# Kernel tuning notes

Measured on AMD Instinct MI355X. Metric: run time of the kernel, lower is better.

## Reference

```python
import jax, jax.numpy as jnp
import numpy as np

D = 1024
ITERATIONS = 2


def setup_inputs() -> dict:
    key = jax.random.key(0)
    ks = jax.random.split(key, 7)
    s = 1.0 / np.sqrt(D)  # PyTorch GRUCell/Linear init scale
    x = jax.random.normal(ks[0], (8, 4096, D), dtype=jnp.float32)
    W_ih = jax.random.uniform(ks[1], (3 * D, D), minval=-s, maxval=s, dtype=jnp.float32)
    W_hh = jax.random.uniform(ks[2], (3 * D, D), minval=-s, maxval=s, dtype=jnp.float32)
    b_ih = jax.random.uniform(ks[3], (3 * D,), minval=-s, maxval=s, dtype=jnp.float32)
    b_hh = jax.random.uniform(ks[4], (3 * D,), minval=-s, maxval=s, dtype=jnp.float32)
    We = jax.random.uniform(ks[5], (1, D), minval=-s, maxval=s, dtype=jnp.float32)
    be = jax.random.uniform(ks[6], (1,), minval=-s, maxval=s, dtype=jnp.float32)
    return {"x": x, "W_ih": W_ih, "W_hh": W_hh, "b_ih": b_ih, "b_hh": b_hh, "We": We, "be": be}


def _gru_cell(inp, h, W_ih, W_hh, b_ih, b_hh):
    # PyTorch GRUCell gate order: r, z, n
    gi = inp @ W_ih.T + b_ih  # [N, 3D]
    gh = h @ W_hh.T + b_hh    # [N, 3D]
    i_r, i_z, i_n = jnp.split(gi, 3, axis=-1)
    h_r, h_z, h_n = jnp.split(gh, 3, axis=-1)
    r = jax.nn.sigmoid(i_r + h_r)
    z = jax.nn.sigmoid(i_z + h_z)
    n = jnp.tanh(i_n + r * h_n)
    return (1.0 - z) * n + z * h


def reference(x, W_ih, W_hh, b_ih, b_hh, We, be):
    B, S, Dm = x.shape
    state = x.reshape(-1, Dm)  # [B*S, D]
    for _ in range(ITERATIONS):
        error = jax.nn.sigmoid(state @ We.T + be)  # [B*S, 1]
        new_state = _gru_cell(state, state, W_ih, W_hh, b_ih, b_hh)
        state = (1.0 - error) * state + error * new_state
    return state.reshape(B, S, Dm)
```

## Files before the change

kernel.cpp:

```cpp
#include <hip/hip_runtime.h>

#define DD 1024

typedef int   i32x4  __attribute__((ext_vector_type(4)));
typedef int   i32x8  __attribute__((ext_vector_type(8)));
typedef float f32x16 __attribute__((ext_vector_type(16)));

__device__ __forceinline__ float sigm(float x) { return 1.0f / (1.0f + __expf(-x)); }
__device__ __forceinline__ float tanh_fast(float x) {
  float e = __expf(-2.0f * fabsf(x));
  float t = (1.0f - e) / (1.0f + e);
  return copysignf(t, x);
}
__device__ __forceinline__ void gload_lds16(const void* g, void* l) {
  __builtin_amdgcn_global_load_lds((const __attribute__((address_space(1))) void*)g,
                                   (__attribute__((address_space(3))) void*)l, 16, 0, 0);
}
__device__ __forceinline__ unsigned pk_fp8x4(float a, float b, float c, float d) {
  int u = __builtin_amdgcn_cvt_pk_fp8_f32(a, b, 0, false);
  u = __builtin_amdgcn_cvt_pk_fp8_f32(c, d, u, true);
  return (unsigned)u;
}


__global__ __launch_bounds__(256) void prep_weights(
    const float* __restrict__ Wih, const float* __restrict__ Whh,
    const float* __restrict__ bih, const float* __restrict__ bhh,
    unsigned char* __restrict__ Wcat8, float* __restrict__ bias) {
  int i = blockIdx.x * 256 + threadIdx.x;
  int g = i >> 18;
  int rem = i & 262143;
  int n = rem >> 8;
  int k4 = rem & 255;
  const float4* wih4 = reinterpret_cast<const float4*>(Wih);
  const float4* whh4 = reinterpret_cast<const float4*>(Whh);
  float4 v;
  if (g == 0) {
    size_t idx = (size_t)n * 256 + k4;
    float4 a = wih4[idx], b = whh4[idx];
    v = make_float4(a.x + b.x, a.y + b.y, a.z + b.z, a.w + b.w);
  } else if (g == 1) {
    size_t idx = (size_t)(DD + n) * 256 + k4;
    float4 a = wih4[idx], b = whh4[idx];
    v = make_float4(a.x + b.x, a.y + b.y, a.z + b.z, a.w + b.w);
  } else if (g == 2) {
    size_t idx = (size_t)(2 * DD + n) * 256 + k4;
    v = wih4[idx];
  } else {
    size_t idx = (size_t)(2 * DD + n) * 256 + k4;
    v = whh4[idx];
  }
  unsigned pkd = pk_fp8x4(v.x * 32.0f, v.y * 32.0f, v.z * 32.0f, v.w * 32.0f);

  int db   = n >> 5;
  int dgl  = n & 31;
  int kt   = k4 >> 4;
  int gran = (k4 >> 2) & 3;
  int sel  = ((gran & 1) << 1) | (gran >> 1);
  int klo  = (k4 & 3) * 4;
  size_t addr = (size_t)db * 131072 + (size_t)kt * 8192 + g * 2048 +
                sel * 512 + dgl * 16 + klo;
  *reinterpret_cast<unsigned*>(Wcat8 + addr) = pkd;

  if (i < 4 * DD) {
    int bg = i >> 10, bn = i & 1023;
    float bv;
    if (bg == 0)      bv = bih[bn] + bhh[bn];
    else if (bg == 1) bv = bih[DD + bn] + bhh[DD + bn];
    else if (bg == 2) bv = bih[2 * DD + bn];
    else              bv = bhh[2 * DD + bn];
    bias[i] = bv;
  }
}

__global__ __launch_bounds__(256) void error_cast(
    const float* S, const float* __restrict__ We, const float* __restrict__ be,
    unsigned char* __restrict__ Sb8, float* __restrict__ err) {
  __shared__ float part[4];
  const int row = blockIdx.x;
  const int t = threadIdx.x;
  float4 v = reinterpret_cast<const float4*>(S + (size_t)row * DD)[t];
  float4 w = reinterpret_cast<const float4*>(We)[t];
  float dot = v.x * w.x + v.y * w.y + v.z * w.z + v.w * w.w;

  int r    = row & 127;
  int kt   = t >> 4;
  int gran = (t >> 2) & 3;
  int sel  = ((gran & 1) << 1) | (gran >> 1);
  int klo  = (t & 3) * 4;
  size_t addr = (size_t)(row >> 7) * 131072 + (size_t)kt * 8192 +
                (r >> 5) * 2048 + sel * 512 + (r & 31) * 16 + klo;
  *reinterpret_cast<unsigned*>(Sb8 + addr) = pk_fp8x4(v.x, v.y, v.z, v.w);

#pragma unroll
  for (int off = 32; off > 0; off >>= 1) dot += __shfl_xor(dot, off);
  if ((t & 63) == 0) part[t >> 6] = dot;
  __syncthreads();
  if (t == 0) err[row] = sigm(part[0] + part[1] + part[2] + part[3] + be[0]);
}

__global__ __launch_bounds__(256, 2) void gru_fused_gemm(
    const unsigned char* __restrict__ Sb8,
    const unsigned char* __restrict__ Wcat8,
    const float* __restrict__ bias,
    const float* __restrict__ err,
    const float* Sf,
    float* out, int M) {
  __shared__ alignas(16) unsigned char Bs[2 * 8192];

  const int bid = blockIdx.x;
  const int x = bid & 7;
  const int c = bid >> 3;
  const int db = (x & 1) * 16 + (c & 15);
  const int mb = (x >> 1) * 32 + (c >> 4);

  const int tid = threadIdx.x;
  const int w = tid >> 6;
  const int lane = tid & 63;
  const int l31 = lane & 31;
  const int h = lane >> 5;

  const unsigned char* sB0 = Wcat8 + (size_t)db * 131072 + (size_t)w * 1024 + lane * 16;
  unsigned char* const dB0 = Bs + w * 1024;

  const unsigned char* aptr[2];
#pragma unroll
  for (int f = 0; f < 2; ++f) {
    int rg = 2 * w + f;
    aptr[f] = Sb8 + (size_t)(2 * mb + (rg >> 2)) * 131072 +
              (rg & 3) * 2048 + h * 512 + l31 * 16;
  }
  const int bq = h * 512 + l31 * 16;

  f32x16 acc[2][4];
#pragma unroll
  for (int f = 0; f < 2; ++f)
#pragma unroll
    for (int g = 0; g < 4; ++g)
#pragma unroll
      for (int r = 0; r < 16; ++r) acc[f][g][r] = 0.0f;

  i32x8 aX[2], aY[2];

#define LOAD_A(T, DST)                                                         \
  {                                                                            \
    _Pragma("unroll")                                                          \
    for (int f = 0; f < 2; ++f) {                                              \
      const unsigned char* p = aptr[f] + (size_t)(T) * 8192;                   \
      i32x4 lo = *reinterpret_cast<const i32x4*>(p);                           \
      i32x4 hi = *reinterpret_cast<const i32x4*>(p + 1024);                    \
      DST[f] = __builtin_shufflevector(lo, hi, 0, 1, 2, 3, 4, 5, 6, 7);        \
    }                                                                          \
  }

  auto stageB = [&](int t) {
    const int slot = (t & 1) * 8192;
    const size_t koff = (size_t)t * 8192;
    gload_lds16(sB0 + koff, dB0 + slot);
    gload_lds16(sB0 + koff + 4096, dB0 + slot + 4096);
  };

  LOAD_A(0, aX)
  stageB(0);
  stageB(1);

#pragma unroll
  for (int t = 0; t < 16; ++t) {
    if (t < 15) asm volatile("s_waitcnt vmcnt(2)" ::: "memory");
    else        asm volatile("s_waitcnt vmcnt(0)" ::: "memory");
    __builtin_amdgcn_s_barrier();

    if (t <= 14) {
      if ((t & 1) == 0) LOAD_A(t + 1, aY)
      else              LOAD_A(t + 1, aX)
    }

    const int sb = (t & 1) * 8192;
    i32x8 bf[4];
#pragma unroll
    for (int g = 0; g < 4; ++g) {
      i32x4 b0 = *reinterpret_cast<const i32x4*>(Bs + sb + g * 2048 + bq);
      i32x4 b1 = *reinterpret_cast<const i32x4*>(Bs + sb + g * 2048 + bq + 1024);
      bf[g] = __builtin_shufflevector(b0, b1, 0, 1, 2, 3, 4, 5, 6, 7);
    }
    asm volatile("s_waitcnt lgkmcnt(0)" ::: "memory");
    __builtin_amdgcn_s_barrier();

    if (t <= 13) stageB(t + 2);

    asm volatile("" ::: "memory");
    __builtin_amdgcn_s_setprio(1);
    if ((t & 1) == 0) {
#pragma unroll
      for (int g = 0; g < 4; ++g)
#pragma unroll
        for (int f = 0; f < 2; ++f)
          acc[f][g] = __builtin_amdgcn_mfma_scale_f32_32x32x64_f8f6f4(
              aX[f], bf[g], acc[f][g], 0, 0, 0, 127, 0, 122);
    } else {
#pragma unroll
      for (int g = 0; g < 4; ++g)
#pragma unroll
        for (int f = 0; f < 2; ++f)
          acc[f][g] = __builtin_amdgcn_mfma_scale_f32_32x32x64_f8f6f4(
              aY[f], bf[g], acc[f][g], 0, 0, 0, 127, 0, 122);
    }
    __builtin_amdgcn_s_setprio(0);
  }
#undef LOAD_A

  const int dgcol = db * 32 + l31;
  const float b_r = bias[dgcol];
  const float b_z = bias[DD + dgcol];
  const float b_i = bias[2 * DD + dgcol];
  const float b_h = bias[3 * DD + dgcol];
#pragma unroll
  for (int f = 0; f < 2; ++f) {
#pragma unroll
    for (int reg = 0; reg < 16; ++reg) {
      int rowf = (reg & 3) + 8 * (reg >> 2) + 4 * h;
      int m = mb * 256 + w * 64 + f * 32 + rowf;
      float e = err[m];
      float hh = Sf[(size_t)m * DD + dgcol];
      float r = sigm(acc[f][0][reg] + b_r);
      float z = sigm(acc[f][1][reg] + b_z);
      float n = tanh_fast(acc[f][2][reg] + b_i + r * (acc[f][3][reg] + b_h));
      out[(size_t)m * DD + dgcol] = hh + e * (1.0f - z) * (n - hh);
    }
  }
}

extern "C" void kernel_launch(void* const* d_in, const int* in_sizes, int n_in,
                              void* d_out, int out_size, void* d_ws, size_t ws_size,
                              hipStream_t stream) {
  const float* x   = (const float*)d_in[0];
  const float* Wih = (const float*)d_in[1];
  const float* Whh = (const float*)d_in[2];
  const float* bih = (const float*)d_in[3];
  const float* bhh = (const float*)d_in[4];
  const float* We  = (const float*)d_in[5];
  const float* be  = (const float*)d_in[6];
  float* out = (float*)d_out;
  const int M = in_sizes[0] / DD;

  char* ws = (char*)d_ws;
  unsigned char* Sb8   = (unsigned char*)ws;
  unsigned char* Wcat8 = (unsigned char*)(ws + (size_t)M * DD);
  float* bias = (float*)(ws + (size_t)M * DD + (size_t)4 * DD * DD);
  float* err  = (float*)(ws + (size_t)M * DD + (size_t)4 * DD * DD + (size_t)4 * DD * 4);

  prep_weights<<<4096, 256, 0, stream>>>(Wih, Whh, bih, bhh, Wcat8, bias);

  const int nwg = (M / 256) * 32;
  const float* S = x;
  for (int it = 0; it < 2; ++it) {
    error_cast<<<M, 256, 0, stream>>>(S, We, be, Sb8, err);
    gru_fused_gemm<<<nwg, 256, 0, stream>>>(Sb8, Wcat8, bias, err, S, out, M);
    S = out;
  }
}
```

Measured before the change: 479.9 us.

## Stage A tiles through LDS with async global_load_lds and raise occupancy

```diff
diff --git a/kernel.cpp b/kernel.cpp
--- a/kernel.cpp
+++ b/kernel.cpp
@@ -99,13 +99,14 @@
   if (t == 0) err[row] = sigm(part[0] + part[1] + part[2] + part[3] + be[0]);
 }
 
-__global__ __launch_bounds__(256, 2) void gru_fused_gemm(
+__global__ __launch_bounds__(256, 3) void gru_fused_gemm(
     const unsigned char* __restrict__ Sb8,
     const unsigned char* __restrict__ Wcat8,
     const float* __restrict__ bias,
     const float* __restrict__ err,
     const float* Sf,
     float* out, int M) {
+  __shared__ alignas(16) unsigned char As[2 * 16384];
   __shared__ alignas(16) unsigned char Bs[2 * 8192];
 
   const int bid = blockIdx.x;
@@ -120,15 +121,22 @@
   const int l31 = lane & 31;
   const int h = lane >> 5;
 
+  const unsigned char* srcA[4];
+  unsigned char* dstA[4];
+#pragma unroll
+  for (int i = 0; i < 4; ++i) {
+    int j = w + i * 4;
+    srcA[i] = Sb8 + (size_t)(2 * mb + (j >> 3)) * 131072 + (j & 7) * 1024 + lane * 16;
+    dstA[i] = As + j * 1024;
+  }
   const unsigned char* sB0 = Wcat8 + (size_t)db * 131072 + (size_t)w * 1024 + lane * 16;
   unsigned char* const dB0 = Bs + w * 1024;
 
-  const unsigned char* aptr[2];
+  int aoff[2];
 #pragma unroll
   for (int f = 0; f < 2; ++f) {
     int rg = 2 * w + f;
-    aptr[f] = Sb8 + (size_t)(2 * mb + (rg >> 2)) * 131072 +
-              (rg & 3) * 2048 + h * 512 + l31 * 16;
+    aoff[f] = (rg >> 2) * 8192 + (rg & 3) * 2048 + h * 512 + l31 * 16;
   }
   const int bq = h * 512 + l31 * 16;
 
@@ -140,74 +148,52 @@
 #pragma unroll
       for (int r = 0; r < 16; ++r) acc[f][g][r] = 0.0f;
 
-  i32x8 aX[2], aY[2];
-
-#define LOAD_A(T, DST)                                                         \
-  {                                                                            \
-    _Pragma("unroll")                                                          \
-    for (int f = 0; f < 2; ++f) {                                              \
-      const unsigned char* p = aptr[f] + (size_t)(T) * 8192;                   \
-      i32x4 lo = *reinterpret_cast<const i32x4*>(p);                           \
-      i32x4 hi = *reinterpret_cast<const i32x4*>(p + 1024);                    \
-      DST[f] = __builtin_shufflevector(lo, hi, 0, 1, 2, 3, 4, 5, 6, 7);        \
-    }                                                                          \
-  }
-
-  auto stageB = [&](int t) {
-    const int slot = (t & 1) * 8192;
+  auto stage = [&](int t) {
     const size_t koff = (size_t)t * 8192;
-    gload_lds16(sB0 + koff, dB0 + slot);
-    gload_lds16(sB0 + koff + 4096, dB0 + slot + 4096);
+    const int sA = (t & 1) * 16384;
+    const int sB = (t & 1) * 8192;
+#pragma unroll
+    for (int i = 0; i < 4; ++i) gload_lds16(srcA[i] + koff, dstA[i] + sA);
+    gload_lds16(sB0 + koff, dB0 + sB);
+    gload_lds16(sB0 + koff + 4096, dB0 + sB + 4096);
   };
 
-  LOAD_A(0, aX)
-  stageB(0);
-  stageB(1);
+  stage(0);
+  stage(1);
 
 #pragma unroll
   for (int t = 0; t < 16; ++t) {
-    if (t < 15) asm volatile("s_waitcnt vmcnt(2)" ::: "memory");
+    const int sA = (t & 1) * 16384;
+    const int sB = (t & 1) * 8192;
+    if (t < 15) asm volatile("s_waitcnt vmcnt(6)" ::: "memory");
     else        asm volatile("s_waitcnt vmcnt(0)" ::: "memory");
     __builtin_amdgcn_s_barrier();
 
-    if (t <= 14) {
-      if ((t & 1) == 0) LOAD_A(t + 1, aY)
-      else              LOAD_A(t + 1, aX)
+    i32x8 a[2];
+#pragma unroll
+    for (int f = 0; f < 2; ++f) {
+      i32x4 a0 = *reinterpret_cast<const i32x4*>(As + sA + aoff[f]);
+      i32x4 a1 = *reinterpret_cast<const i32x4*>(As + sA + aoff[f] + 1024);
+      a[f] = __builtin_shufflevector(a0, a1, 0, 1, 2, 3, 4, 5, 6, 7);
     }
 
-    const int sb = (t & 1) * 8192;
-    i32x8 bf[4];
+    __builtin_amdgcn_s_setprio(1);
 #pragma unroll
     for (int g = 0; g < 4; ++g) {
-      i32x4 b0 = *reinterpret_cast<const i32x4*>(Bs + sb + g * 2048 + bq);
-      i32x4 b1 = *reinterpret_cast<const i32x4*>(Bs + sb + g * 2048 + bq + 1024);
-      bf[g] = __builtin_shufflevector(b0, b1, 0, 1, 2, 3, 4, 5, 6, 7);
+      i32x4 b0 = *reinterpret_cast<const i32x4*>(Bs + sB + g * 2048 + bq);
+      i32x4 b1 = *reinterpret_cast<const i32x4*>(Bs + sB + g * 2048 + bq + 1024);
+      i32x8 bf = __builtin_shufflevector(b0, b1, 0, 1, 2, 3, 4, 5, 6, 7);
+      acc[0][g] = __builtin_amdgcn_mfma_scale_f32_32x32x64_f8f6f4(
+          a[0], bf, acc[0][g], 0, 0, 0, 127, 0, 122);
+      acc[1][g] = __builtin_amdgcn_mfma_scale_f32_32x32x64_f8f6f4(
+          a[1], bf, acc[1][g], 0, 0, 0, 127, 0, 122);
     }
+    __builtin_amdgcn_s_setprio(0);
+
     asm volatile("s_waitcnt lgkmcnt(0)" ::: "memory");
     __builtin_amdgcn_s_barrier();
-
-    if (t <= 13) stageB(t + 2);
-
-    asm volatile("" ::: "memory");
-    __builtin_amdgcn_s_setprio(1);
-    if ((t & 1) == 0) {
-#pragma unroll
-      for (int g = 0; g < 4; ++g)
-#pragma unroll
-        for (int f = 0; f < 2; ++f)
-          acc[f][g] = __builtin_amdgcn_mfma_scale_f32_32x32x64_f8f6f4(
-              aX[f], bf[g], acc[f][g], 0, 0, 0, 127, 0, 122);
-    } else {
-#pragma unroll
-      for (int g = 0; g < 4; ++g)
-#pragma unroll
-        for (int f = 0; f < 2; ++f)
-          acc[f][g] = __builtin_amdgcn_mfma_scale_f32_32x32x64_f8f6f4(
-              aY[f], bf[g], acc[f][g], 0, 0, 0, 127, 0, 122);
-    }
-    __builtin_amdgcn_s_setprio(0);
-  }
-#undef LOAD_A
+    if (t <= 13) stage(t + 2);
+  }
 
   const int dgcol = db * 32 + l31;
   const float b_r = bias[dgcol];
```

Result: faster. 453.9 us (-5.4%).
